# Kernel optimization log

Measured on AMD Instinct MI355X. Metric: run time of the kernel, lower is better.

The kernel has to match this reference:

```python
import jax, jax.numpy as jnp
import numpy as np

NUM_HEADS = 16
HEAD_DIM = 64
HIDDEN = NUM_HEADS * HEAD_DIM
LN_EPS = 1e-6


def setup_inputs() -> dict:
    key = jax.random.key(0)
    ks = jax.random.split(key, 5)
    B, T, H = 2, 2048, HIDDEN
    s = 1.0 / np.sqrt(H)
    return {
        "h": jax.random.normal(ks[0], (B, T, H), jnp.float32),
        "Wq": jax.random.normal(ks[1], (H, H), jnp.float32) * s,
        "bq": jnp.zeros((H,), jnp.float32),
        "Wk": jax.random.normal(ks[2], (H, H), jnp.float32) * s,
        "bk": jnp.zeros((H,), jnp.float32),
        "Wv": jax.random.normal(ks[3], (H, H), jnp.float32) * s,
        "bv": jnp.zeros((H,), jnp.float32),
        "Wo": jax.random.normal(ks[4], (H, H), jnp.float32) * s,
        "bo": jnp.zeros((H,), jnp.float32),
        "gamma": jnp.ones((H,), jnp.float32),
        "beta": jnp.zeros((H,), jnp.float32),
    }


def _split_heads(x):
    B, T, H = x.shape
    return x.reshape(B, T, NUM_HEADS, HEAD_DIM).transpose(0, 2, 1, 3)  # [B,h,T,d]


def reference(h, Wq, bq, Wk, bk, Wv, bv, Wo, bo, gamma, beta):
    # QKV projections (nn.Linear: x @ W^T + b)
    Q = _split_heads(h @ Wq.T + bq)
    K = _split_heads(h @ Wk.T + bk)
    V = _split_heads(h @ Wv.T + bv)
    scale = HEAD_DIM ** -0.5
    scores = jnp.einsum("bhqd,bhkd->bhqk", Q, K) * scale  # [B,h,T,T]
    attn = jax.nn.softmax(scores, axis=-1)
    ctx = jnp.einsum("bhqk,bhkd->bhqd", attn, V)          # [B,h,T,d]
    B, _, T, _ = ctx.shape
    ctx = ctx.transpose(0, 2, 1, 3).reshape(B, T, HIDDEN)
    out = ctx @ Wo.T + bo + h  # dropout is identity at eval
    # LayerNorm(eps=1e-6)
    mu = out.mean(-1, keepdims=True)
    var = jnp.mean((out - mu) ** 2, -1, keepdims=True)
    return (out - mu) * jax.lax.rsqrt(var + LN_EPS) * gamma + beta
```

## Files before the change

kernel.cpp:

```cpp
#include <hip/hip_runtime.h>
#include <hip/hip_bf16.h>

#define NH   16
#define HD   64
#define HID  1024
#define TSEQ 2048
#define BATCH 2
#define KSCALE 0.18033688011112042f

typedef __attribute__((ext_vector_type(4))) float f32x4;
typedef __attribute__((ext_vector_type(8))) short s16x8;
typedef __attribute__((ext_vector_type(4))) short s16x4;
typedef __attribute__((ext_vector_type(8))) _Float16 f16x8;
typedef __attribute__((ext_vector_type(4))) _Float16 f16x4;
typedef __attribute__((ext_vector_type(2))) _Float16 f16x2;

__device__ __forceinline__ unsigned short f2bf(float f) {
  union { float f; unsigned int u; } v; v.f = f;
  unsigned int r = v.u + 0x7fffu + ((v.u >> 16) & 1u);
  return (unsigned short)(r >> 16);
}
__device__ __forceinline__ float bf2f(unsigned short b) {
  union { unsigned int u; float f; } v; v.u = ((unsigned int)b) << 16; return v.f;
}

__device__ __forceinline__ void async_cp16(const unsigned short* g, unsigned short* l) {
  __builtin_amdgcn_global_load_lds(
      (const __attribute__((address_space(1))) unsigned int*)g,
      (__attribute__((address_space(3))) unsigned int*)l, 16, 0, 0);
}

__global__ __launch_bounds__(256) void cast_all_k(
    const float* __restrict__ h,
    const float* __restrict__ w0, const float* __restrict__ w1,
    const float* __restrict__ w2, const float* __restrict__ w3,
    unsigned short* __restrict__ hb, unsigned short* __restrict__ wbase) {
  int i = blockIdx.x * 256 + threadIdx.x;
  const float* src; unsigned short* dst; int idx; float sc = 1.f;
  if (i < 1048576) { src = h; dst = hb; idx = i; }
  else {
    int idx4 = i - 1048576;
    int w = idx4 >> 18;
    idx = idx4 & 262143;
    src = (w == 0) ? w0 : (w == 1) ? w1 : (w == 2) ? w2 : w3;
    dst = wbase + (size_t)(idx4 - idx) * 4;
    if (w == 1) sc = KSCALE;
  }
  float4 v = ((const float4*)src)[idx];
  ushort4 o;
  o.x = f2bf(v.x * sc); o.y = f2bf(v.y * sc); o.z = f2bf(v.z * sc); o.w = f2bf(v.w * sc);
  ((ushort4*)dst)[idx] = o;
}

__global__ __launch_bounds__(256) void gemm_qkv(
    const unsigned short* __restrict__ hb,
    const unsigned short* __restrict__ wq, const unsigned short* __restrict__ wk,
    const unsigned short* __restrict__ wv,
    const float* __restrict__ bq, const float* __restrict__ bk, const float* __restrict__ bv,
    unsigned short* __restrict__ qo, unsigned short* __restrict__ ko,
    unsigned short* __restrict__ vto) {
  __shared__ unsigned short Ash[128 * 32];
  __shared__ unsigned short Bsh[64 * 32];
  const unsigned short* Bw; const float* bias; float bsc = 1.f;
  if (blockIdx.z == 0)      { Bw = wq; bias = bq; }
  else if (blockIdx.z == 1) { Bw = wk; bias = bk; bsc = KSCALE; }
  else                      { Bw = wv; bias = bv; }
  const int tid = threadIdx.x, lane = tid & 63, wave = tid >> 6;
  const int l15 = lane & 15, quad = lane >> 4;
  const int wm = (wave >> 1) * 64, wn = (wave & 1) * 32;
  const int bm = blockIdx.y * 128, bn = blockIdx.x * 64;
  const unsigned short* Ag = hb + (size_t)bm * HID;
  const unsigned short* Bg = Bw + (size_t)bn * HID;
  const int idx0 = tid * 8, idx1 = idx0 + 2048;
  const int r0 = idx0 >> 5, c0 = idx0 & 31;
  const int r1 = idx1 >> 5, c1 = idx1 & 31;
  f32x4 acc[4][2];
#pragma unroll
  for (int i = 0; i < 4; ++i)
#pragma unroll
    for (int j = 0; j < 2; ++j) acc[i][j] = f32x4{0.f, 0.f, 0.f, 0.f};

  for (int k0 = 0; k0 < HID; k0 += 32) {
    __syncthreads();
    async_cp16(Ag + r0 * HID + k0 + c0, Ash + idx0);
    async_cp16(Ag + r1 * HID + k0 + c1, Ash + idx1);
    async_cp16(Bg + r0 * HID + k0 + c0, Bsh + idx0);
    __syncthreads();
    s16x8 af[4], bfr[2];
#pragma unroll
    for (int i = 0; i < 4; ++i)
      af[i] = *(const s16x8*)(Ash + (wm + i * 16 + l15) * 32 + quad * 8);
#pragma unroll
    for (int j = 0; j < 2; ++j)
      bfr[j] = *(const s16x8*)(Bsh + (wn + j * 16 + l15) * 32 + quad * 8);
#pragma unroll
    for (int i = 0; i < 4; ++i)
#pragma unroll
      for (int j = 0; j < 2; ++j)
        acc[i][j] = __builtin_amdgcn_mfma_f32_16x16x32_bf16(af[i], bfr[j], acc[i][j], 0, 0, 0);
  }

  if (blockIdx.z == 2) {
#pragma unroll
    for (int j = 0; j < 2; ++j) {
      const int col = bn + wn + j * 16 + l15;
      const float bb = bias[col];
      const int head = col >> 6, d = col & 63;
#pragma unroll
      for (int i = 0; i < 4; ++i) {
        const int row0 = bm + wm + i * 16 + quad * 4;
        const int bI = row0 >> 11, t0 = row0 & 2047;
        unsigned short o[4];
#pragma unroll
        for (int r = 0; r < 4; ++r) {
          _Float16 hv = (_Float16)(acc[i][j][r] + bb);
          o[r] = __builtin_bit_cast(unsigned short, hv);
        }
        *(s16x4*)(vto + ((size_t)((bI * NH + head) * HD + d)) * TSEQ + t0) = *(const s16x4*)o;
      }
    }
  } else {
    unsigned short* outp = (blockIdx.z == 0) ? qo : ko;
#pragma unroll
    for (int j = 0; j < 2; ++j) {
      const int col = bn + wn + j * 16 + l15;
      const float bb = bias[col] * bsc;
      const int head = col >> 6, d = col & 63;
#pragma unroll
      for (int i = 0; i < 4; ++i) {
#pragma unroll
        for (int r = 0; r < 4; ++r) {
          const int row = bm + wm + i * 16 + quad * 4 + r;
          const int bI = row >> 11, t = row & 2047;
          outp[(((size_t)(bI * NH + head) * TSEQ) + t) * HD + d] = f2bf(acc[i][j][r] + bb);
        }
      }
    }
  }
}

__global__ __launch_bounds__(256) void gemm_out(
    const unsigned short* __restrict__ ctx, const unsigned short* __restrict__ wo,
    const float* __restrict__ bo, const float* __restrict__ hres,
    float* __restrict__ outf) {
  __shared__ unsigned short Ash[128 * 32];
  __shared__ unsigned short Bsh[64 * 32];
  const int tid = threadIdx.x, lane = tid & 63, wave = tid >> 6;
  const int l15 = lane & 15, quad = lane >> 4;
  const int wm = (wave >> 1) * 64, wn = (wave & 1) * 32;
  const int bm = blockIdx.y * 128, bn = blockIdx.x * 64;
  const unsigned short* Ag = ctx + (size_t)bm * HID;
  const unsigned short* Bg = wo + (size_t)bn * HID;
  const int idx0 = tid * 8, idx1 = idx0 + 2048;
  const int r0 = idx0 >> 5, c0 = idx0 & 31;
  const int r1 = idx1 >> 5, c1 = idx1 & 31;
  f32x4 acc[4][2];
#pragma unroll
  for (int i = 0; i < 4; ++i)
#pragma unroll
    for (int j = 0; j < 2; ++j) acc[i][j] = f32x4{0.f, 0.f, 0.f, 0.f};

  for (int k0 = 0; k0 < HID; k0 += 32) {
    __syncthreads();
    async_cp16(Ag + r0 * HID + k0 + c0, Ash + idx0);
    async_cp16(Ag + r1 * HID + k0 + c1, Ash + idx1);
    async_cp16(Bg + r0 * HID + k0 + c0, Bsh + idx0);
    __syncthreads();
    s16x8 af[4], bfr[2];
#pragma unroll
    for (int i = 0; i < 4; ++i)
      af[i] = *(const s16x8*)(Ash + (wm + i * 16 + l15) * 32 + quad * 8);
#pragma unroll
    for (int j = 0; j < 2; ++j)
      bfr[j] = *(const s16x8*)(Bsh + (wn + j * 16 + l15) * 32 + quad * 8);
#pragma unroll
    for (int i = 0; i < 4; ++i)
#pragma unroll
      for (int j = 0; j < 2; ++j)
        acc[i][j] = __builtin_amdgcn_mfma_f32_16x16x32_bf16(af[i], bfr[j], acc[i][j], 0, 0, 0);
  }
#pragma unroll
  for (int j = 0; j < 2; ++j) {
    const int col = bn + wn + j * 16 + l15;
    const float bb = bo[col];
#pragma unroll
    for (int i = 0; i < 4; ++i) {
#pragma unroll
      for (int r = 0; r < 4; ++r) {
        const int row = bm + wm + i * 16 + quad * 4 + r;
        const size_t off = (size_t)row * HID + col;
        outf[off] = acc[i][j][r] + bb + hres[off];
      }
    }
  }
}

__global__ __launch_bounds__(256, 2) void attn_k(
    const unsigned short* __restrict__ qb, const unsigned short* __restrict__ kb,
    const unsigned short* __restrict__ vt, unsigned short* __restrict__ ctx,
    unsigned short* __restrict__ Opart, float* __restrict__ rsumP,
    int lsplit, int ntiles) {
  __shared__ unsigned short Ksh[64 * 72];
  __shared__ unsigned short Vsh[64 * 72];

  const int tid = threadIdx.x, lane = tid & 63, wave = tid >> 6;
  const int l15 = lane & 15, quad = lane >> 4;
  const int z = blockIdx.z;
  const int b = z >> lsplit;
  const int part = z & ((1 << lsplit) - 1);
  const int h = blockIdx.y, qt = blockIdx.x;
  const size_t ho = ((size_t)(b * NH + h)) * TSEQ * HD;
  const unsigned short* Qh = qb + ho;
  const unsigned short* Kh = kb + ho;
  const unsigned short* Vh = vt + ho;
  const int q0 = qt * 128 + wave * 32;
  const int kt0 = part * ntiles;

  s16x8 qf[2][2];
#pragma unroll
  for (int s = 0; s < 2; ++s)
#pragma unroll
    for (int ks = 0; ks < 2; ++ks)
      qf[s][ks] = *(const s16x8*)(Qh + (size_t)(q0 + s * 16 + l15) * HD + ks * 32 + quad * 8);

  f32x4 accO[4][2];
  float rsum[2];
#pragma unroll
  for (int n2 = 0; n2 < 4; ++n2)
#pragma unroll
    for (int s = 0; s < 2; ++s) accO[n2][s] = f32x4{0.f, 0.f, 0.f, 0.f};
  rsum[0] = rsum[1] = 0.f;

  const int sr = tid >> 3, sc = (tid & 7) * 8;
  s16x8 kreg[2], vreg[2];
#pragma unroll
  for (int hf = 0; hf < 2; ++hf) {
    kreg[hf] = *(const s16x8*)(Kh + (size_t)(kt0 * 64 + sr + hf * 32) * HD + sc);
    vreg[hf] = *(const s16x8*)(Vh + (size_t)(sr + hf * 32) * TSEQ + kt0 * 64 + sc);
  }

  for (int kt = 0; kt < ntiles; ++kt) {
    __syncthreads();
#pragma unroll
    for (int hf = 0; hf < 2; ++hf) {
      *(s16x8*)(Ksh + (sr + hf * 32) * 72 + sc) = kreg[hf];
      *(s16x8*)(Vsh + (sr + hf * 32) * 72 + sc) = vreg[hf];
    }
    __syncthreads();
    if (kt + 1 < ntiles) {
      const int k0n = (kt0 + kt + 1) * 64;
#pragma unroll
      for (int hf = 0; hf < 2; ++hf) {
        kreg[hf] = *(const s16x8*)(Kh + (size_t)(k0n + sr + hf * 32) * HD + sc);
        vreg[hf] = *(const s16x8*)(Vh + (size_t)(sr + hf * 32) * TSEQ + k0n + sc);
      }
    }

    f32x4 accS[2][4];
#pragma unroll
    for (int s = 0; s < 2; ++s)
#pragma unroll
      for (int n = 0; n < 4; ++n) accS[s][n] = f32x4{0.f, 0.f, 0.f, 0.f};
#pragma unroll
    for (int ks = 0; ks < 2; ++ks) {
#pragma unroll
      for (int n = 0; n < 4; ++n) {
        s16x8 kf = *(const s16x8*)(Ksh + (n * 16 + l15) * 72 + ks * 32 + quad * 8);
#pragma unroll
        for (int s = 0; s < 2; ++s)
          accS[s][n] = __builtin_amdgcn_mfma_f32_16x16x32_bf16(kf, qf[s][ks], accS[s][n], 0, 0, 0);
      }
    }

    f16x4 pB[2][4];
#pragma unroll
    for (int s = 0; s < 2; ++s)
#pragma unroll
      for (int n = 0; n < 4; ++n) {
        float e0 = __builtin_amdgcn_exp2f(accS[s][n][0]);
        float e1 = __builtin_amdgcn_exp2f(accS[s][n][1]);
        float e2 = __builtin_amdgcn_exp2f(accS[s][n][2]);
        float e3 = __builtin_amdgcn_exp2f(accS[s][n][3]);
        rsum[s] += (e0 + e1) + (e2 + e3);
        f16x2 lo = __builtin_bit_cast(f16x2, __builtin_amdgcn_cvt_pkrtz(e0, e1));
        f16x2 hi = __builtin_bit_cast(f16x2, __builtin_amdgcn_cvt_pkrtz(e2, e3));
        pB[s][n] = f16x4{lo[0], lo[1], hi[0], hi[1]};
      }

#pragma unroll
    for (int n = 0; n < 4; ++n) {
#pragma unroll
      for (int n2 = 0; n2 < 4; ++n2) {
        f16x4 vA = *(const f16x4*)(Vsh + (n2 * 16 + l15) * 72 + n * 16 + quad * 4);
#pragma unroll
        for (int s = 0; s < 2; ++s)
          accO[n2][s] = __builtin_amdgcn_mfma_f32_16x16x16f16(vA, pB[s][n], accO[n2][s], 0, 0, 0);
      }
    }
  }

#pragma unroll
  for (int s = 0; s < 2; ++s) {
    float t = rsum[s];
    t += __shfl_xor(t, 16, 64);
    t += __shfl_xor(t, 32, 64);
    rsum[s] = t;
  }

  if (lsplit) {
    const int slot = (part * BATCH + b) * NH + h;
    const size_t ob = (size_t)slot * TSEQ * HD;
#pragma unroll
    for (int s = 0; s < 2; ++s) {
      const int t = q0 + s * 16 + l15;
#pragma unroll
      for (int n2 = 0; n2 < 4; ++n2) {
        const int d0 = n2 * 16 + quad * 4;
        unsigned short o[4];
#pragma unroll
        for (int r = 0; r < 4; ++r) o[r] = f2bf(accO[n2][s][r]);
        *(s16x4*)(Opart + ob + (size_t)t * HD + d0) = *(const s16x4*)o;
      }
    }
    if (quad == 0) {
      const size_t rb = (size_t)slot * TSEQ;
#pragma unroll
      for (int s = 0; s < 2; ++s)
        rsumP[rb + q0 + s * 16 + l15] = rsum[s];
    }
  } else {
#pragma unroll
    for (int s = 0; s < 2; ++s) {
      const int t = q0 + s * 16 + l15;
      const float inv = 1.f / rsum[s];
#pragma unroll
      for (int n2 = 0; n2 < 4; ++n2) {
        const int d0 = n2 * 16 + quad * 4;
        unsigned short o[4];
#pragma unroll
        for (int r = 0; r < 4; ++r) o[r] = f2bf(accO[n2][s][r] * inv);
        *(s16x4*)(ctx + ((size_t)(b * TSEQ + t)) * HID + h * HD + d0) = *(const s16x4*)o;
      }
    }
  }
}

__global__ __launch_bounds__(256) void combine_k(
    const unsigned short* __restrict__ Opart, const float* __restrict__ rsumP,
    unsigned short* __restrict__ ctx, int nparts) {
  const int gtid = blockIdx.x * 256 + threadIdx.x;
  const int d = (gtid & 7) * 8;
  const int rem = gtid >> 3;
  const int t = rem & 2047;
  const int bh = rem >> 11;
  float acc[8] = {0, 0, 0, 0, 0, 0, 0, 0};
  float rs = 0.f;
  for (int p = 0; p < nparts; ++p) {
    const int slot = p * 32 + bh;
    s16x8 a = *(const s16x8*)(Opart + ((size_t)slot * TSEQ + t) * HD + d);
#pragma unroll
    for (int j = 0; j < 8; ++j) acc[j] += bf2f(((const unsigned short*)&a)[j]);
    rs += rsumP[(size_t)slot * TSEQ + t];
  }
  const float inv = 1.f / rs;
  unsigned short o[8];
#pragma unroll
  for (int j = 0; j < 8; ++j) o[j] = f2bf(acc[j] * inv);
  const int b = bh >> 4, h = bh & 15;
  *(s16x8*)(ctx + ((size_t)(b * TSEQ + t)) * HID + h * HD + d) = *(const s16x8*)o;
}

__global__ __launch_bounds__(256) void ln_k(float* __restrict__ io,
                                            const float* __restrict__ gamma,
                                            const float* __restrict__ beta) {
  const int row = blockIdx.x, tid = threadIdx.x;
  float x[4]; float s = 0.f, s2 = 0.f;
#pragma unroll
  for (int i = 0; i < 4; ++i) {
    x[i] = io[(size_t)row * HID + tid + i * 256];
    s += x[i]; s2 += x[i] * x[i];
  }
#pragma unroll
  for (int off = 1; off < 64; off <<= 1) {
    s  += __shfl_xor(s, off, 64);
    s2 += __shfl_xor(s2, off, 64);
  }
  __shared__ float red[8];
  const int wave = tid >> 6;
  if ((tid & 63) == 0) { red[wave] = s; red[wave + 4] = s2; }
  __syncthreads();
  s  = red[0] + red[1] + red[2] + red[3];
  s2 = red[4] + red[5] + red[6] + red[7];
  const float mean = s * (1.f / HID);
  const float var  = s2 * (1.f / HID) - mean * mean;
  const float rstd = rsqrtf(var + 1e-6f);
#pragma unroll
  for (int i = 0; i < 4; ++i) {
    const int col = tid + i * 256;
    io[(size_t)row * HID + col] = (x[i] - mean) * rstd * gamma[col] + beta[col];
  }
}

extern "C" void kernel_launch(void* const* d_in, const int* in_sizes, int n_in,
                              void* d_out, int out_size, void* d_ws, size_t ws_size,
                              hipStream_t stream) {
  const float* h    = (const float*)d_in[0];
  const float* Wq   = (const float*)d_in[1];
  const float* bq   = (const float*)d_in[2];
  const float* Wk   = (const float*)d_in[3];
  const float* bk   = (const float*)d_in[4];
  const float* Wv   = (const float*)d_in[5];
  const float* bv   = (const float*)d_in[6];
  const float* Wo   = (const float*)d_in[7];
  const float* bo   = (const float*)d_in[8];
  const float* gamma = (const float*)d_in[9];
  const float* beta  = (const float*)d_in[10];
  float* out = (float*)d_out;

  unsigned short* hb   = (unsigned short*)d_ws;
  unsigned short* wqb  = hb  + 4194304;
  unsigned short* wkb  = wqb + 1048576;
  unsigned short* wvb  = wkb + 1048576;
  unsigned short* wob  = wvb + 1048576;
  unsigned short* qb   = wob + 1048576;
  unsigned short* kb   = qb  + 4194304;
  unsigned short* vtf  = kb  + 4194304;
  unsigned short* Opart = vtf + 4194304;
  unsigned short* ctxb = hb;

  const size_t base = (size_t)(vtf + 4194304 - hb) * 2;
  int lsplit = 0;
  if (ws_size >= base + 2u * 8388608 + 2u * 262144) lsplit = 1;
  const int nparts = 1 << lsplit;
  float* rsumP = (float*)(Opart + (size_t)nparts * 4194304);

  cast_all_k<<<8192, 256, 0, stream>>>(h, Wq, Wk, Wv, Wo, hb, wqb);
  gemm_qkv<<<dim3(16, 32, 3), 256, 0, stream>>>(hb, wqb, wkb, wvb, bq, bk, bv, qb, kb, vtf);
  attn_k<<<dim3(TSEQ / 128, NH, BATCH << lsplit), 256, 0, stream>>>(
      qb, kb, vtf, ctxb, Opart, rsumP, lsplit, 32 >> lsplit);
  if (lsplit)
    combine_k<<<2048, 256, 0, stream>>>(Opart, rsumP, ctxb, nparts);
  gemm_out<<<dim3(16, 32), 256, 0, stream>>>(ctxb, wob, bo, h, out);
  ln_k<<<4096, 256, 0, stream>>>(out, gamma, beta);
}
```

Baseline: 226.1 us.

## Fuse Q/K/V projections into one GEMM block sharing the activation tile

The QKV GEMM now has each block load one 64x32 activation tile and three 64x32 weight tiles (Wq, Wk, Wv), computing all three projections together instead of using a separate grid z-slice per projection. This removes the triple reload of the activation tile from global memory and the per-z branching. In exchange the block tile shrinks from 128x64 to 64x64 per output, so each weight tile is reused across fewer rows. The grid grows from 16x32x3 to 16x64 blocks, and each wave now holds 12 accumulators.

```diff
diff --git a/kernel.cpp b/kernel.cpp
--- a/kernel.cpp
+++ b/kernel.cpp
@@ -59,82 +59,84 @@
     const float* __restrict__ bq, const float* __restrict__ bk, const float* __restrict__ bv,
     unsigned short* __restrict__ qo, unsigned short* __restrict__ ko,
     unsigned short* __restrict__ vto) {
-  __shared__ unsigned short Ash[128 * 32];
-  __shared__ unsigned short Bsh[64 * 32];
-  const unsigned short* Bw; const float* bias; float bsc = 1.f;
-  if (blockIdx.z == 0)      { Bw = wq; bias = bq; }
-  else if (blockIdx.z == 1) { Bw = wk; bias = bk; bsc = KSCALE; }
-  else                      { Bw = wv; bias = bv; }
+  __shared__ unsigned short Ash[64 * 32];
+  __shared__ unsigned short Bsh[3][64 * 32];
   const int tid = threadIdx.x, lane = tid & 63, wave = tid >> 6;
   const int l15 = lane & 15, quad = lane >> 4;
-  const int wm = (wave >> 1) * 64, wn = (wave & 1) * 32;
-  const int bm = blockIdx.y * 128, bn = blockIdx.x * 64;
+  const int wn = wave * 16;
+  const int bm = blockIdx.y * 64, bn = blockIdx.x * 64;
   const unsigned short* Ag = hb + (size_t)bm * HID;
-  const unsigned short* Bg = Bw + (size_t)bn * HID;
-  const int idx0 = tid * 8, idx1 = idx0 + 2048;
-  const int r0 = idx0 >> 5, c0 = idx0 & 31;
-  const int r1 = idx1 >> 5, c1 = idx1 & 31;
-  f32x4 acc[4][2];
-#pragma unroll
-  for (int i = 0; i < 4; ++i)
-#pragma unroll
-    for (int j = 0; j < 2; ++j) acc[i][j] = f32x4{0.f, 0.f, 0.f, 0.f};
+  const unsigned short* Bg0 = wq + (size_t)bn * HID;
+  const unsigned short* Bg1 = wk + (size_t)bn * HID;
+  const unsigned short* Bg2 = wv + (size_t)bn * HID;
+  const int idx = tid * 8;
+  const int rA = idx >> 5, cA = idx & 31;
+
+  f32x4 acc[3][4];
+#pragma unroll
+  for (int m = 0; m < 3; ++m)
+#pragma unroll
+    for (int i = 0; i < 4; ++i) acc[m][i] = f32x4{0.f, 0.f, 0.f, 0.f};
 
   for (int k0 = 0; k0 < HID; k0 += 32) {
     __syncthreads();
-    async_cp16(Ag + r0 * HID + k0 + c0, Ash + idx0);
-    async_cp16(Ag + r1 * HID + k0 + c1, Ash + idx1);
-    async_cp16(Bg + r0 * HID + k0 + c0, Bsh + idx0);
-    __syncthreads();
-    s16x8 af[4], bfr[2];
+    async_cp16(Ag  + rA * HID + k0 + cA, Ash    + idx);
+    async_cp16(Bg0 + rA * HID + k0 + cA, Bsh[0] + idx);
+    async_cp16(Bg1 + rA * HID + k0 + cA, Bsh[1] + idx);
+    async_cp16(Bg2 + rA * HID + k0 + cA, Bsh[2] + idx);
+    __syncthreads();
+    s16x8 af[4];
 #pragma unroll
     for (int i = 0; i < 4; ++i)
-      af[i] = *(const s16x8*)(Ash + (wm + i * 16 + l15) * 32 + quad * 8);
-#pragma unroll
-    for (int j = 0; j < 2; ++j)
-      bfr[j] = *(const s16x8*)(Bsh + (wn + j * 16 + l15) * 32 + quad * 8);
-#pragma unroll
-    for (int i = 0; i < 4; ++i)
-#pragma unroll
-      for (int j = 0; j < 2; ++j)
-        acc[i][j] = __builtin_amdgcn_mfma_f32_16x16x32_bf16(af[i], bfr[j], acc[i][j], 0, 0, 0);
-  }
-
-  if (blockIdx.z == 2) {
-#pragma unroll
-    for (int j = 0; j < 2; ++j) {
-      const int col = bn + wn + j * 16 + l15;
-      const float bb = bias[col];
-      const int head = col >> 6, d = col & 63;
-#pragma unroll
-      for (int i = 0; i < 4; ++i) {
-        const int row0 = bm + wm + i * 16 + quad * 4;
-        const int bI = row0 >> 11, t0 = row0 & 2047;
-        unsigned short o[4];
-#pragma unroll
-        for (int r = 0; r < 4; ++r) {
-          _Float16 hv = (_Float16)(acc[i][j][r] + bb);
-          o[r] = __builtin_bit_cast(unsigned short, hv);
-        }
-        *(s16x4*)(vto + ((size_t)((bI * NH + head) * HD + d)) * TSEQ + t0) = *(const s16x4*)o;
-      }
-    }
-  } else {
-    unsigned short* outp = (blockIdx.z == 0) ? qo : ko;
-#pragma unroll
-    for (int j = 0; j < 2; ++j) {
-      const int col = bn + wn + j * 16 + l15;
-      const float bb = bias[col] * bsc;
-      const int head = col >> 6, d = col & 63;
-#pragma unroll
-      for (int i = 0; i < 4; ++i) {
-#pragma unroll
-        for (int r = 0; r < 4; ++r) {
-          const int row = bm + wm + i * 16 + quad * 4 + r;
-          const int bI = row >> 11, t = row & 2047;
-          outp[(((size_t)(bI * NH + head) * TSEQ) + t) * HD + d] = f2bf(acc[i][j][r] + bb);
-        }
-      }
+      af[i] = *(const s16x8*)(Ash + (i * 16 + l15) * 32 + quad * 8);
+#pragma unroll
+    for (int m = 0; m < 3; ++m) {
+      s16x8 bfr = *(const s16x8*)(Bsh[m] + (wn + l15) * 32 + quad * 8);
+#pragma unroll
+      for (int i = 0; i < 4; ++i)
+        acc[m][i] = __builtin_amdgcn_mfma_f32_16x16x32_bf16(af[i], bfr, acc[m][i], 0, 0, 0);
+    }
+  }
+
+  const int col = bn + wn + l15;
+  const int head = col >> 6, d = col & 63;
+  {
+    const float bb = bq[col];
+#pragma unroll
+    for (int i = 0; i < 4; ++i) {
+#pragma unroll
+      for (int r = 0; r < 4; ++r) {
+        const int row = bm + i * 16 + quad * 4 + r;
+        const int bI = row >> 11, t = row & 2047;
+        qo[(((size_t)(bI * NH + head) * TSEQ) + t) * HD + d] = f2bf(acc[0][i][r] + bb);
+      }
+    }
+  }
+  {
+    const float bb = bk[col] * KSCALE;
+#pragma unroll
+    for (int i = 0; i < 4; ++i) {
+#pragma unroll
+      for (int r = 0; r < 4; ++r) {
+        const int row = bm + i * 16 + quad * 4 + r;
+        const int bI = row >> 11, t = row & 2047;
+        ko[(((size_t)(bI * NH + head) * TSEQ) + t) * HD + d] = f2bf(acc[1][i][r] + bb);
+      }
+    }
+  }
+  {
+    const float bb = bv[col];
+#pragma unroll
+    for (int i = 0; i < 4; ++i) {
+      const int row0 = bm + i * 16 + quad * 4;
+      const int bI = row0 >> 11, t0 = row0 & 2047;
+      unsigned short o[4];
+#pragma unroll
+      for (int r = 0; r < 4; ++r) {
+        _Float16 hv = (_Float16)(acc[2][i][r] + bb);
+        o[r] = __builtin_bit_cast(unsigned short, hv);
+      }
+      *(s16x4*)(vto + ((size_t)((bI * NH + head) * HD + d)) * TSEQ + t0) = *(const s16x4*)o;
     }
   }
 }
@@ -435,7 +437,7 @@
   float* rsumP = (float*)(Opart + (size_t)nparts * 4194304);
 
   cast_all_k<<<8192, 256, 0, stream>>>(h, Wq, Wk, Wv, Wo, hb, wqb);
-  gemm_qkv<<<dim3(16, 32, 3), 256, 0, stream>>>(hb, wqb, wkb, wvb, bq, bk, bv, qb, kb, vtf);
+  gemm_qkv<<<dim3(16, 64), 256, 0, stream>>>(hb, wqb, wkb, wvb, bq, bk, bv, qb, kb, vtf);
   attn_k<<<dim3(TSEQ / 128, NH, BATCH << lsplit), 256, 0, stream>>>(
       qb, kb, vtf, ctxb, Opart, rsumP, lsplit, 32 >> lsplit);
   if (lsplit)
```

New measurement: 220.8 us. 2.4% less time.
